# Optimization experiments

Hardware: AMD Instinct MI355X
Metric: run time of the kernel (lower is better)

Reference implementation:

```python
import jax, jax.numpy as jnp
import numpy as np

# --- static config (matches init_kwargs) ---
T, V, D, H = 4096, 32000, 1024, 16
DH = D // H                      # rope/head dim = 64
E, CAP, K, HOPS = 8, 1024, 2, 3  # non-identity experts, capacity, top-k, hops
MLP = 4 * D
ROPE_BASE = 10000.0
ATTN_IDX = np.array([0, 2, 4, 6])  # experts built with i%2==0 -> Attention
FFN_IDX = np.array([1, 3, 5, 7])   # i%2==1 -> FeedForward
EPS = 1e-6


def rope_cos_sin(t, dh, base):
    inv = 1.0 / (base ** (jnp.arange(0, dh, 2, dtype=jnp.float32) / dh))
    ang = jnp.arange(t, dtype=jnp.float32)[:, None] * inv[None, :]  # [T, dh/2]
    ang = jnp.concatenate([ang, ang], axis=-1)                      # [T, dh]
    return jnp.cos(ang), jnp.sin(ang)


def rotate_half(x):
    h = x.shape[-1] // 2
    return jnp.concatenate([-x[..., h:], x[..., :h]], axis=-1)


def topk_mask(logits, k):
    # boolean [T, E_total] mask of per-row top-k
    _, idx = jax.lax.top_k(logits, k)
    hard = jax.nn.one_hot(idx, logits.shape[-1]).sum(axis=-2)
    return hard.astype(bool)


def capacity_select(mask_te, gate_te, capacity):
    # mask_te: [T,E] bool, gate_te: [T,E] float -> slot [E,C,T], kept [E,T]
    m = mask_te.T                                   # [E, T]
    g = jnp.where(m, gate_te.T, -jnp.inf)           # [E, T]
    cap = int(min(capacity, g.shape[1]))
    _, top_idx = jax.lax.top_k(g, cap)              # [E, C]
    Ee, C = top_idx.shape
    slot = jnp.zeros((Ee, C, g.shape[1]), g.dtype)
    slot = slot.at[jnp.arange(Ee)[:, None], jnp.arange(C)[None, :], top_idx].set(1.0)
    slot = slot * m[:, None, :]                     # drop -inf fill slots
    kept = slot.sum(1).astype(bool)                 # [E, T]
    return slot, kept


def rms_norm(x, w):
    return x * jax.lax.rsqrt(jnp.mean(x * x, axis=-1, keepdims=True) + EPS) * w


def attention_group(x, cos_r, sin_r, wq, wk, wv, wo):
    # x: [G,C,D]; cos_r/sin_r: [G,C,DH]; weights: [G,D,D]
    G, C, _ = x.shape
    q = jnp.einsum('gcd,gde->gce', x, wq).reshape(G, C, H, DH)
    k = jnp.einsum('gcd,gde->gce', x, wk).reshape(G, C, H, DH)
    v = jnp.einsum('gcd,gde->gce', x, wv).reshape(G, C, H, DH)
    c = cos_r[:, :, None, :]
    s = sin_r[:, :, None, :]
    q = q * c + rotate_half(q) * s
    k = k * c + rotate_half(k) * s
    scores = jnp.einsum('gqhd,gkhd->ghqk', q, k) / np.sqrt(DH).astype(np.float32)
    attn = jax.nn.softmax(scores, axis=-1)
    out = jnp.einsum('ghqk,gkhd->gqhd', attn, v).reshape(G, C, D)
    return jnp.einsum('gcd,gde->gce', out, wo)


def ffn_group(x, w1, w2):
    # x: [G,C,D]; w1: [G,D,MLP]; w2: [G,MLP,D]
    return jnp.einsum('gcf,gfd->gcd', jax.nn.gelu(jnp.einsum('gcd,gdf->gcf', x, w1)), w2)


def dna_forward(ids, embed_w, router_w, wq, wk, wv, wo, w1, w2, ln_w):
    h = embed_w[ids]                                     # [T, D]
    cos, sin = rope_cos_sin(T, DH, ROPE_BASE)            # [T, DH]
    for hop in range(HOPS):
        logits = h @ router_w[hop].T                     # [T, E+1]
        probs = jax.nn.softmax(logits, axis=-1)
        mask_full = topk_mask(logits, K)                 # [T, E+1]
        probs_tr = probs[:, :-1]                         # [T, E]
        mask_tr = mask_full[:, :-1]
        slot, kept = capacity_select(mask_tr, probs_tr, CAP)  # [E,C,T], [E,T]
        # dispatch
        xin = jnp.einsum('ect,td->ecd', slot, h)          # [E, C, D]
        cos_r = jnp.einsum('ect,td->ecd', slot, cos)      # [E, C, DH]
        sin_r = jnp.einsum('ect,td->ecd', slot, sin)
        # grouped expert execution (stacked params, vectorized over group dim)
        attn_out = attention_group(xin[ATTN_IDX], cos_r[ATTN_IDX], sin_r[ATTN_IDX],
                                   wq, wk, wv, wo)        # [4, C, D]
        ffn_out = ffn_group(xin[FFN_IDX], w1, w2)         # [4, C, D]
        expert_out = jnp.zeros((E, CAP, D), h.dtype)
        expert_out = expert_out.at[ATTN_IDX].set(attn_out).at[FFN_IDX].set(ffn_out)
        # combine
        combine_w = jnp.where(kept.T, probs_tr, 0.0)      # [T, E]
        rho = combine_w.sum(axis=1, keepdims=True)        # [T, 1]
        combine = jnp.einsum('ecd,ect,et->td', expert_out, slot, combine_w.T)
        h = h + combine - rho * h
    return rms_norm(h, ln_w)


def setup_inputs() -> dict:
    key = jax.random.key(0)
    ks = jax.random.split(key, 10)
    sc = 0.02
    return {
        'ids': jax.random.randint(ks[0], (T,), 0, V),
        'embed_w': jax.random.normal(ks[1], (V, D), jnp.float32) * sc,
        'router_w': jax.random.normal(ks[2], (HOPS, E + 1, D), jnp.float32) * sc,
        'wq': jax.random.normal(ks[3], (4, D, D), jnp.float32) * sc,
        'wk': jax.random.normal(ks[4], (4, D, D), jnp.float32) * sc,
        'wv': jax.random.normal(ks[5], (4, D, D), jnp.float32) * sc,
        'wo': jax.random.normal(ks[6], (4, D, D), jnp.float32) * sc,
        'w1': jax.random.normal(ks[7], (4, D, MLP), jnp.float32) * sc,
        'w2': jax.random.normal(ks[8], (4, MLP, D), jnp.float32) * sc,
        'ln_w': jnp.ones((D,), jnp.float32),
    }


def reference(ids, embed_w, router_w, wq, wk, wv, wo, w1, w2, ln_w):
    return dna_forward(ids, embed_w, router_w, wq, wk, wv, wo, w1, w2, ln_w)
```

## Files before the change

kernel.cpp:

```cpp
#include <hip/hip_runtime.h>
#include <math.h>

#define T_ 4096
#define D_ 1024
#define H_ 16
#define DH_ 64
#define E_ 8
#define CAP_ 1024
#define MLP_ 4096
#define HOPS_ 3

__global__ __launch_bounds__(256) void embed_kernel(
    const int* __restrict__ ids, const float* __restrict__ ew, float* __restrict__ h)
{
  const int t = blockIdx.x;
  const int id = ids[t];
  const int c = threadIdx.x * 4;
  *(float4*)(h + (size_t)t * D_ + c) = *(const float4*)(ew + (size_t)id * D_ + c);
}

__global__ __launch_bounds__(64) void router_kernel(
    const float* __restrict__ h, const float* __restrict__ rw,
    float* __restrict__ probs, float* __restrict__ gmask)
{
  const int t = blockIdx.x;
  const int lane = threadIdx.x;
  __shared__ float hs[D_];
  #pragma unroll
  for (int j = 0; j < 4; ++j)
    *(float4*)&hs[lane * 4 + j * 256] = *(const float4*)(h + (size_t)t * D_ + lane * 4 + j * 256);
  __syncthreads();
  float l9[9];
  #pragma unroll
  for (int e = 0; e < 9; ++e) {
    float s = 0.0f;
    for (int i = lane; i < D_; i += 64) s += hs[i] * rw[e * D_ + i];
    #pragma unroll
    for (int off = 32; off > 0; off >>= 1) s += __shfl_down(s, off);
    l9[e] = s;
  }
  if (lane == 0) {
    float m = l9[0];
    #pragma unroll
    for (int e = 1; e < 9; ++e) m = fmaxf(m, l9[e]);
    float sum = 0.0f;
    float ex[9];
    #pragma unroll
    for (int e = 0; e < 9; ++e) { ex[e] = expf(l9[e] - m); sum += ex[e]; }
    const float inv = 1.0f / sum;
    int b1 = 0;
    #pragma unroll
    for (int e = 1; e < 9; ++e) if (l9[e] > l9[b1]) b1 = e;
    int b2 = (b1 == 0) ? 1 : 0;
    #pragma unroll
    for (int e = 0; e < 9; ++e) if (e != b1 && e != b2 && l9[e] > l9[b2]) b2 = e;
    #pragma unroll
    for (int e = 0; e < 8; ++e) {
      const float pe = ex[e] * inv;
      probs[t * 8 + e] = pe;
      gmask[(size_t)e * T_ + t] = (e == b1 || e == b2) ? pe : -1e30f;
    }
  }
}

__global__ __launch_bounds__(256) void zero_kernel(float* __restrict__ rho, int* __restrict__ cnt)
{
  const int i = blockIdx.x * 256 + threadIdx.x;
  if (i < T_) rho[i] = 0.0f;
  if (i < E_) cnt[i] = 0;
}

__global__ __launch_bounds__(256) void zeroeo_kernel(float* __restrict__ eo)
{
  const size_t i = ((size_t)blockIdx.x * 256 + threadIdx.x) * 4;
  float4 z; z.x = z.y = z.z = z.w = 0.0f;
  *(float4*)(eo + i) = z;
}

__global__ __launch_bounds__(256) void select_kernel(
    const float* __restrict__ gmask, const float* __restrict__ probs,
    int* __restrict__ idx, int* __restrict__ cnt, float* __restrict__ rho)
{
  __shared__ float row[T_];
  const int e = blockIdx.y;
  const int tid = threadIdx.x;
  const float* gr = gmask + (size_t)e * T_;
  #pragma unroll
  for (int j = 0; j < 16; ++j) row[tid + 256 * j] = gr[tid + 256 * j];
  __syncthreads();
  const int t = blockIdx.x * 256 + tid;
  const float g = row[t];
  if (g > -1e29f) {
    int rank = 0;
    for (int tt = 0; tt < T_; ++tt) {
      const float gg = row[tt];
      rank += (gg > g) || (gg == g && tt < t);
    }
    if (rank < CAP_) {
      const int pos = atomicAdd(&cnt[e], 1);
      idx[e * CAP_ + pos] = t;
      atomicAdd(&rho[t], probs[t * 8 + e]);
    }
  }
}

typedef __bf16 bf16x8 __attribute__((ext_vector_type(8)));
typedef float f32x4v __attribute__((ext_vector_type(4)));

union FragU { uint2 u2[2]; bf16x8 v; };

__device__ __forceinline__ unsigned pack_hi2(unsigned u0, unsigned u1)
{
  return (u0 >> 16) | (u1 & 0xFFFF0000u);
}

__device__ __forceinline__ void split8(const float4 a, const float4 b, FragU& h, FragU& l)
{
  const float f[8] = {a.x, a.y, a.z, a.w, b.x, b.y, b.z, b.w};
  unsigned hu[8], lu[8];
  #pragma unroll
  for (int i = 0; i < 8; ++i) {
    const unsigned u = __float_as_uint(f[i]);
    const float lo = f[i] - __uint_as_float(u & 0xFFFF0000u);
    hu[i] = u; lu[i] = __float_as_uint(lo);
  }
  h.u2[0].x = pack_hi2(hu[0], hu[1]); h.u2[0].y = pack_hi2(hu[2], hu[3]);
  h.u2[1].x = pack_hi2(hu[4], hu[5]); h.u2[1].y = pack_hi2(hu[6], hu[7]);
  l.u2[0].x = pack_hi2(lu[0], lu[1]); l.u2[0].y = pack_hi2(lu[2], lu[3]);
  l.u2[1].x = pack_hi2(lu[4], lu[5]); l.u2[1].y = pack_hi2(lu[6], lu[7]);
}

__device__ __forceinline__ void lds_load16(const void* g, void* l)
{
  __builtin_amdgcn_global_load_lds(
      (const __attribute__((address_space(1))) unsigned int*)g,
      (__attribute__((address_space(3))) unsigned int*)l, 16, 0, 0);
}

__device__ __forceinline__ float gelu_tanh(float x)
{
  const float x3 = x * x * x;
  return 0.5f * x * (1.0f + tanhf(0.7978845608028654f * (x + 0.044715f * x3)));
}

__global__ __launch_bounds__(256) void gather_kernel(
    const float* __restrict__ h, const int* __restrict__ idx, const int* __restrict__ cnt,
    unsigned short* __restrict__ xinp)
{
  const int c = blockIdx.x, e = blockIdx.y;
  const int c4 = threadIdx.x * 4;
  unsigned short* dst = xinp + ((size_t)e * CAP_ + c) * 2 * D_;
  if (c < cnt[e]) {
    const int t = idx[e * CAP_ + c];
    const float4 x = *(const float4*)(h + (size_t)t * D_ + c4);
    const float f[4] = {x.x, x.y, x.z, x.w};
    unsigned hu[4], lu[4];
    #pragma unroll
    for (int j = 0; j < 4; ++j) {
      const unsigned u = __float_as_uint(f[j]);
      const float lo = f[j] - __uint_as_float(u & 0xFFFF0000u);
      hu[j] = u; lu[j] = __float_as_uint(lo);
    }
    uint2 hp, lp;
    hp.x = pack_hi2(hu[0], hu[1]); hp.y = pack_hi2(hu[2], hu[3]);
    lp.x = pack_hi2(lu[0], lu[1]); lp.y = pack_hi2(lu[2], lu[3]);
    *(uint2*)(dst + c4) = hp;
    *(uint2*)(dst + D_ + c4) = lp;
  } else {
    uint2 z; z.x = 0u; z.y = 0u;
    *(uint2*)(dst + c4) = z;
    *(uint2*)(dst + D_ + c4) = z;
  }
}

__global__ __launch_bounds__(256) void convw_kernel(
    const float* __restrict__ W, unsigned short* __restrict__ out, int K, int N)
{
  const float* Wp = W + (size_t)blockIdx.z * K * N;
  unsigned short* op = out + (size_t)blockIdx.z * N * 2 * K;
  const int k0 = blockIdx.y * 64, n0 = blockIdx.x * 64;
  __shared__ float tile[64][65];
  const int tr = threadIdx.x >> 6;
  const int tc = threadIdx.x & 63;
  #pragma unroll
  for (int it = 0; it < 16; ++it) {
    const int r = it * 4 + tr;
    tile[r][tc] = Wp[(size_t)(k0 + r) * N + n0 + tc];
  }
  __syncthreads();
  #pragma unroll
  for (int it = 0; it < 16; ++it) {
    const int n = it * 4 + tr;
    const float f = tile[tc][n];
    const unsigned u = __float_as_uint(f);
    const float lo = f - __uint_as_float(u & 0xFFFF0000u);
    op[(size_t)(n0 + n) * 2 * K + k0 + tc] = (unsigned short)(u >> 16);
    op[(size_t)(n0 + n) * 2 * K + K + k0 + tc] = (unsigned short)(__float_as_uint(lo) >> 16);
  }
}

template <int EPI>
__device__ __forceinline__ void gemm_bf16_core(
    const unsigned short* __restrict__ A, const unsigned short* __restrict__ B,
    void* __restrict__ Cv, int N, int K, int kc0, int nkc, int m0, int n0)
{
  __shared__ unsigned short As[128 * 64];
  __shared__ unsigned short Bs[128 * 64];

  const int tid = threadIdx.x;
  const int lane = tid & 63;
  const int w = tid >> 6;
  const int wm = w >> 1, wn = w & 1;
  const int quad = lane >> 4, l15 = lane & 15;
  const size_t K2 = (size_t)2 * K;

  f32x4v acc[4][4];
  #pragma unroll
  for (int i = 0; i < 4; ++i)
    #pragma unroll
    for (int j = 0; j < 4; ++j) { acc[i][j][0] = 0.f; acc[i][j][1] = 0.f; acc[i][j][2] = 0.f; acc[i][j][3] = 0.f; }

  const int r0 = tid >> 3;
  const int pc = tid & 7;

  for (int kc = kc0; kc < kc0 + nkc; ++kc) {
    const int kb = kc * 32;
    __syncthreads();
    #pragma unroll
    for (int i = 0; i < 4; ++i) {
      const int row = r0 + i * 32;
      const int lc = pc ^ (row & 7);
      const int goff = (lc < 4) ? (kb + lc * 8) : (K + kb + (lc - 4) * 8);
      lds_load16(A + (size_t)(m0 + row) * K2 + goff, &As[(tid + i * 256) * 8]);
    }
    #pragma unroll
    for (int i = 0; i < 4; ++i) {
      const int row = r0 + i * 32;
      const int lc = pc ^ (row & 7);
      const int goff = (lc < 4) ? (kb + lc * 8) : (K + kb + (lc - 4) * 8);
      lds_load16(B + (size_t)(n0 + row) * K2 + goff, &Bs[(tid + i * 256) * 8]);
    }
    __syncthreads();

    FragU fah[4], fbh[4], fbl[4], fal[4];
    #pragma unroll
    for (int i = 0; i < 4; ++i) {
      const int row = wm * 64 + i * 16 + l15;
      const unsigned short* pr = &As[row * 64 + ((quad ^ (row & 7)) * 8)];
      fah[i].u2[0] = *(const uint2*)pr; fah[i].u2[1] = *(const uint2*)(pr + 4);
    }
    #pragma unroll
    for (int j = 0; j < 4; ++j) {
      const int row = wn * 64 + j * 16 + l15;
      const unsigned short* pr = &Bs[row * 64 + ((quad ^ (row & 7)) * 8)];
      fbh[j].u2[0] = *(const uint2*)pr; fbh[j].u2[1] = *(const uint2*)(pr + 4);
    }
    #pragma unroll
    for (int i = 0; i < 4; ++i)
      #pragma unroll
      for (int j = 0; j < 4; ++j)
        acc[i][j] = __builtin_amdgcn_mfma_f32_16x16x32_bf16(fah[i].v, fbh[j].v, acc[i][j], 0, 0, 0);
    #pragma unroll
    for (int j = 0; j < 4; ++j) {
      const int row = wn * 64 + j * 16 + l15;
      const unsigned short* pr = &Bs[row * 64 + (((quad + 4) ^ (row & 7)) * 8)];
      fbl[j].u2[0] = *(const uint2*)pr; fbl[j].u2[1] = *(const uint2*)(pr + 4);
    }
    #pragma unroll
    for (int i = 0; i < 4; ++i)
      #pragma unroll
      for (int j = 0; j < 4; ++j)
        acc[i][j] = __builtin_amdgcn_mfma_f32_16x16x32_bf16(fah[i].v, fbl[j].v, acc[i][j], 0, 0, 0);
    #pragma unroll
    for (int i = 0; i < 4; ++i) {
      const int row = wm * 64 + i * 16 + l15;
      const unsigned short* pr = &As[row * 64 + (((quad + 4) ^ (row & 7)) * 8)];
      fal[i].u2[0] = *(const uint2*)pr; fal[i].u2[1] = *(const uint2*)(pr + 4);
    }
    #pragma unroll
    for (int i = 0; i < 4; ++i)
      #pragma unroll
      for (int j = 0; j < 4; ++j)
        acc[i][j] = __builtin_amdgcn_mfma_f32_16x16x32_bf16(fal[i].v, fbh[j].v, acc[i][j], 0, 0, 0);
  }

  #pragma unroll
  for (int i = 0; i < 4; ++i)
    #pragma unroll
    for (int j = 0; j < 4; ++j) {
      const int n = n0 + wn * 64 + j * 16 + l15;
      #pragma unroll
      for (int r = 0; r < 4; ++r) {
        const int m = m0 + wm * 64 + i * 16 + quad * 4 + r;
        const float v = acc[i][j][r];
        if (EPI == 0) {
          ((float*)Cv)[(size_t)m * N + n] = v;
        } else if (EPI == 2) {
          atomicAdd(&((float*)Cv)[(size_t)m * N + n], v);
        } else {
          const float gv = gelu_tanh(v);
          const unsigned u = __float_as_uint(gv);
          const float lo = gv - __uint_as_float(u & 0xFFFF0000u);
          unsigned short* C = (unsigned short*)Cv;
          C[(size_t)m * 2 * N + n] = (unsigned short)(u >> 16);
          C[(size_t)m * 2 * N + N + n] = (unsigned short)(__float_as_uint(lo) >> 16);
        }
      }
    }
}

template <int EPI, int SK>
__global__ __launch_bounds__(256, 2) void gemm_bf16_k(
    const unsigned short* __restrict__ Ab, const unsigned short* __restrict__ Bb,
    void* __restrict__ Cb, int N, int K, long sA, long sB, long sC)
{
  const int nx = gridDim.x, ny = gridDim.y;
  const int total = nx * ny * gridDim.z;
  int flat = blockIdx.x + nx * (blockIdx.y + ny * blockIdx.z);
  int s = (flat & 7) * (total >> 3) + (flat >> 3);
  const int bx = s % nx; s /= nx;
  const int by = s % ny;
  const int z = s / ny;

  const int g = z / SK, sp = z - g * SK;
  const unsigned short* A = Ab + (size_t)g * sA;
  const unsigned short* B = Bb + (size_t)g * sB;
  void* C;
  if (EPI == 1) C = (void*)((unsigned short*)Cb + (size_t)g * sC);
  else          C = (void*)((float*)Cb + (size_t)g * sC);
  const int nkc = (K / 32) / SK;
  gemm_bf16_core<EPI>(A, B, C, N, K, sp * nkc, nkc, by * 128, bx * 128);
}

__global__ __launch_bounds__(256, 2) void gemm_qkv_bf16(
    const unsigned short* __restrict__ xinp,
    const unsigned short* __restrict__ wqp, const unsigned short* __restrict__ wkp,
    const unsigned short* __restrict__ wvp,
    float* __restrict__ qb, float* __restrict__ kb, float* __restrict__ vb)
{
  const int nx = gridDim.x, ny = gridDim.y;
  const int total = nx * ny * gridDim.z;
  int flat = blockIdx.x + nx * (blockIdx.y + ny * blockIdx.z);
  int s = (flat & 7) * (total >> 3) + (flat >> 3);
  const int bx = s % nx; s /= nx;
  const int by = s % ny;
  const int z = s / ny;

  const int g = z & 3;
  const int which = z >> 2;
  const unsigned short* A = xinp + (size_t)(2 * g) * CAP_ * 2 * D_;
  const unsigned short* B = ((which == 0) ? wqp : (which == 1) ? wkp : wvp) + (size_t)g * D_ * 2 * D_;
  float* C = ((which == 0) ? qb : (which == 1) ? kb : vb) + (size_t)g * CAP_ * D_;
  gemm_bf16_core<0>(A, B, (void*)C, D_, D_, 0, 32, by * 128, bx * 128);
}

__global__ __launch_bounds__(256) void rope_kernel(
    float* __restrict__ q, float* __restrict__ k,
    const int* __restrict__ idx, const int* __restrict__ cnt)
{
  const int c = blockIdx.x, g = blockIdx.y;
  const int e = 2 * g;
  if (c >= cnt[e]) return;
  const int t = idx[e * CAP_ + c];
  const int tid = threadIdx.x;
  const int hh = tid >> 4;
  const int pp = tid & 15;
  const size_t base = ((size_t)g * CAP_ + c) * D_ + hh * DH_;
  const float tf = (float)t;
  #pragma unroll
  for (int u = 0; u < 2; ++u) {
    const int i = pp * 2 + u;
    const float invf = (float)::pow(10000.0, -(double)i / 32.0);
    const float ang = tf * invf;
    const float cs = (float)::cos((double)ang);
    const float sn = (float)::sin((double)ang);
    const float q0 = q[base + i], q1 = q[base + i + 32];
    q[base + i]      = q0 * cs - q1 * sn;
    q[base + i + 32] = q1 * cs + q0 * sn;
    const float k0 = k[base + i], k1 = k[base + i + 32];
    k[base + i]      = k0 * cs - k1 * sn;
    k[base + i + 32] = k1 * cs + k0 * sn;
  }
}

#define FBQ 128
#define LDK 68
#define LDQ 72

__global__ __launch_bounds__(256, 2) void flash_mfma(
    const float* __restrict__ qg, const float* __restrict__ kg,
    const float* __restrict__ vg, unsigned short* __restrict__ og)
{
  const int g = blockIdx.z, hh = blockIdx.y, qt = blockIdx.x;
  const size_t base = (size_t)g * CAP_ * D_ + hh * DH_;
  const float* Q = qg + base;
  const float* Kp = kg + base;
  const float* Vp = vg + base;
  unsigned short* Ob = og + (size_t)g * CAP_ * 2 * D_ + hh * DH_;

  __shared__ __align__(16) char lds_raw[69632];
  unsigned short* Kh  = (unsigned short*)lds_raw;
  unsigned short* Kl  = Kh  + 64 * LDK;
  unsigned short* Vth = Kl  + 64 * LDK;
  unsigned short* Vtl = Vth + 64 * LDK;
  unsigned short* Ph  = Vtl + 64 * LDK;
  unsigned short* Pl  = Ph  + FBQ * LDK;
  float* Qs = (float*)lds_raw;

  const int tid = threadIdx.x;
  const int lane = tid & 63;
  const int w = tid >> 6;
  const int quad = lane >> 4;
  const int l15 = lane & 15;

  #pragma unroll
  for (int it = 0; it < 8; ++it) {
    const int row = it * 16 + (tid >> 4);
    const int c4 = (tid & 15) * 4;
    *(float4*)&Qs[row * LDQ + c4] = *(const float4*)(Q + (size_t)(qt * FBQ + row) * D_ + c4);
  }
  __syncthreads();
  FragU qf[2][2][2];
  #pragma unroll
  for (int rs = 0; rs < 2; ++rs)
    #pragma unroll
    for (int ks = 0; ks < 2; ++ks) {
      const float* p0 = &Qs[(w * 32 + rs * 16 + l15) * LDQ + ks * 32 + quad * 8];
      const float4 f0 = *(const float4*)p0;
      const float4 f1 = *(const float4*)(p0 + 4);
      split8(f0, f1, qf[rs][ks][0], qf[rs][ks][1]);
    }
  __syncthreads();

  f32x4v acc[2][4];
  float m_r[2][4], l_r[2][4];
  #pragma unroll
  for (int rs = 0; rs < 2; ++rs)
    #pragma unroll
    for (int r = 0; r < 4; ++r) { m_r[rs][r] = -1e30f; l_r[rs][r] = 0.0f; }
  #pragma unroll
  for (int rs = 0; rs < 2; ++rs)
    #pragma unroll
    for (int dt = 0; dt < 4; ++dt) { acc[rs][dt][0] = 0.f; acc[rs][dt][1] = 0.f; acc[rs][dt][2] = 0.f; acc[rs][dt][3] = 0.f; }

  for (int kt = 0; kt < 16; ++kt) {
    __syncthreads();
    #pragma unroll
    for (int it = 0; it < 4; ++it) {
      const int r = it * 16 + (tid >> 4);
      const int c4 = (tid & 15) * 4;
      const float4 kv = *(const float4*)(Kp + (size_t)(kt * 64 + r) * D_ + c4);
      {
        const unsigned u0 = __float_as_uint(kv.x), u1 = __float_as_uint(kv.y);
        const unsigned u2 = __float_as_uint(kv.z), u3 = __float_as_uint(kv.w);
        const float l0 = kv.x - __uint_as_float(u0 & 0xFFFF0000u);
        const float l1 = kv.y - __uint_as_float(u1 & 0xFFFF0000u);
        const float l2 = kv.z - __uint_as_float(u2 & 0xFFFF0000u);
        const float l3 = kv.w - __uint_as_float(u3 & 0xFFFF0000u);
        uint2 hp, lp;
        hp.x = pack_hi2(u0, u1); hp.y = pack_hi2(u2, u3);
        lp.x = pack_hi2(__float_as_uint(l0), __float_as_uint(l1));
        lp.y = pack_hi2(__float_as_uint(l2), __float_as_uint(l3));
        *(uint2*)&Kh[r * LDK + c4] = hp;
        *(uint2*)&Kl[r * LDK + c4] = lp;
      }
      const float4 vv = *(const float4*)(Vp + (size_t)(kt * 64 + r) * D_ + c4);
      const float vf[4] = {vv.x, vv.y, vv.z, vv.w};
      #pragma unroll
      for (int u = 0; u < 4; ++u) {
        const unsigned uu = __float_as_uint(vf[u]);
        const float lo = vf[u] - __uint_as_float(uu & 0xFFFF0000u);
        Vth[(c4 + u) * LDK + r] = (unsigned short)(uu >> 16);
        Vtl[(c4 + u) * LDK + r] = (unsigned short)(__float_as_uint(lo) >> 16);
      }
    }
    __syncthreads();
    f32x4v sfr[2][4];
    #pragma unroll
    for (int rs = 0; rs < 2; ++rs)
      #pragma unroll
      for (int j = 0; j < 4; ++j) {
        f32x4v s; s[0] = 0.f; s[1] = 0.f; s[2] = 0.f; s[3] = 0.f;
        #pragma unroll
        for (int ks = 0; ks < 2; ++ks) {
          FragU kh, kl;
          const unsigned short* pk = &Kh[(j * 16 + l15) * LDK + ks * 32 + quad * 8];
          const unsigned short* pl = &Kl[(j * 16 + l15) * LDK + ks * 32 + quad * 8];
          kh.u2[0] = *(const uint2*)pk; kh.u2[1] = *(const uint2*)(pk + 4);
          kl.u2[0] = *(const uint2*)pl; kl.u2[1] = *(const uint2*)(pl + 4);
          s = __builtin_amdgcn_mfma_f32_16x16x32_bf16(qf[rs][ks][0].v, kh.v, s, 0, 0, 0);
          s = __builtin_amdgcn_mfma_f32_16x16x32_bf16(qf[rs][ks][0].v, kl.v, s, 0, 0, 0);
          s = __builtin_amdgcn_mfma_f32_16x16x32_bf16(qf[rs][ks][1].v, kh.v, s, 0, 0, 0);
        }
        sfr[rs][j] = s;
      }
    #pragma unroll
    for (int rs = 0; rs < 2; ++rs) {
      #pragma unroll
      for (int r = 0; r < 4; ++r) {
        float s0 = sfr[rs][0][r] * 0.125f;
        float s1 = sfr[rs][1][r] * 0.125f;
        float s2 = sfr[rs][2][r] * 0.125f;
        float s3 = sfr[rs][3][r] * 0.125f;
        float mx = fmaxf(fmaxf(s0, s1), fmaxf(s2, s3));
        #pragma unroll
        for (int o = 1; o < 16; o <<= 1) mx = fmaxf(mx, __shfl_xor(mx, o));
        const float nm = fmaxf(m_r[rs][r], mx);
        const float al = __expf(m_r[rs][r] - nm);
        m_r[rs][r] = nm;
        const float p0 = __expf(s0 - nm);
        const float p1 = __expf(s1 - nm);
        const float p2 = __expf(s2 - nm);
        const float p3 = __expf(s3 - nm);
        float rsum = p0 + p1 + p2 + p3;
        #pragma unroll
        for (int o = 1; o < 16; o <<= 1) rsum += __shfl_xor(rsum, o);
        l_r[rs][r] = l_r[rs][r] * al + rsum;
        #pragma unroll
        for (int dt = 0; dt < 4; ++dt) acc[rs][dt][r] *= al;
        const int row = w * 32 + rs * 16 + quad * 4 + r;
        const float pv[4] = {p0, p1, p2, p3};
        #pragma unroll
        for (int j = 0; j < 4; ++j) {
          const unsigned u = __float_as_uint(pv[j]);
          const float lo = pv[j] - __uint_as_float(u & 0xFFFF0000u);
          Ph[row * LDK + j * 16 + l15] = (unsigned short)(u >> 16);
          Pl[row * LDK + j * 16 + l15] = (unsigned short)(__float_as_uint(lo) >> 16);
        }
      }
    }
    __syncthreads();
    FragU pf[2][2][2];
    #pragma unroll
    for (int rs = 0; rs < 2; ++rs)
      #pragma unroll
      for (int ks = 0; ks < 2; ++ks) {
        const unsigned short* ph = &Ph[(w * 32 + rs * 16 + l15) * LDK + ks * 32 + quad * 8];
        const unsigned short* pl = &Pl[(w * 32 + rs * 16 + l15) * LDK + ks * 32 + quad * 8];
        pf[rs][ks][0].u2[0] = *(const uint2*)ph; pf[rs][ks][0].u2[1] = *(const uint2*)(ph + 4);
        pf[rs][ks][1].u2[0] = *(const uint2*)pl; pf[rs][ks][1].u2[1] = *(const uint2*)(pl + 4);
      }
    #pragma unroll
    for (int dt = 0; dt < 4; ++dt)
      #pragma unroll
      for (int ks = 0; ks < 2; ++ks) {
        FragU vh, vl;
        const unsigned short* pv_ = &Vth[(dt * 16 + l15) * LDK + ks * 32 + quad * 8];
        const unsigned short* pl_ = &Vtl[(dt * 16 + l15) * LDK + ks * 32 + quad * 8];
        vh.u2[0] = *(const uint2*)pv_; vh.u2[1] = *(const uint2*)(pv_ + 4);
        vl.u2[0] = *(const uint2*)pl_; vl.u2[1] = *(const uint2*)(pl_ + 4);
        #pragma unroll
        for (int rs = 0; rs < 2; ++rs) {
          acc[rs][dt] = __builtin_amdgcn_mfma_f32_16x16x32_bf16(pf[rs][ks][0].v, vh.v, acc[rs][dt], 0, 0, 0);
          acc[rs][dt] = __builtin_amdgcn_mfma_f32_16x16x32_bf16(pf[rs][ks][0].v, vl.v, acc[rs][dt], 0, 0, 0);
          acc[rs][dt] = __builtin_amdgcn_mfma_f32_16x16x32_bf16(pf[rs][ks][1].v, vh.v, acc[rs][dt], 0, 0, 0);
        }
      }
  }
  #pragma unroll
  for (int rs = 0; rs < 2; ++rs)
    #pragma unroll
    for (int r = 0; r < 4; ++r) {
      const float inv = 1.0f / l_r[rs][r];
      const int row = qt * FBQ + w * 32 + rs * 16 + quad * 4 + r;
      #pragma unroll
      for (int dt = 0; dt < 4; ++dt) {
        const float v = acc[rs][dt][r] * inv;
        const unsigned u = __float_as_uint(v);
        const float lo = v - __uint_as_float(u & 0xFFFF0000u);
        Ob[(size_t)row * 2 * D_ + dt * 16 + l15] = (unsigned short)(u >> 16);
        Ob[(size_t)row * 2 * D_ + D_ + dt * 16 + l15] = (unsigned short)(__float_as_uint(lo) >> 16);
      }
    }
}

__global__ __launch_bounds__(256) void initnew_kernel(
    const float* __restrict__ h, const float* __restrict__ rho, float* __restrict__ hn)
{
  const int t = blockIdx.x;
  const float f = 1.0f - rho[t];
  const int c = threadIdx.x * 4;
  float4 x = *(const float4*)(h + (size_t)t * D_ + c);
  x.x *= f; x.y *= f; x.z *= f; x.w *= f;
  *(float4*)(hn + (size_t)t * D_ + c) = x;
}

__global__ __launch_bounds__(256) void scatter_kernel(
    const float* __restrict__ eo, const int* __restrict__ idx, const int* __restrict__ cnt,
    const float* __restrict__ probs, float* __restrict__ hn)
{
  const int c = blockIdx.x, e = blockIdx.y;
  if (c >= cnt[e]) return;
  const int t = idx[e * CAP_ + c];
  const float w = probs[t * 8 + e];
  const float* src = eo + ((size_t)e * CAP_ + c) * D_;
  float* dst = hn + (size_t)t * D_;
  const int c4 = threadIdx.x * 4;
  #pragma unroll
  for (int j = 0; j < 4; ++j) atomicAdd(dst + c4 + j, src[c4 + j] * w);
}

__global__ __launch_bounds__(256) void rms_kernel(
    const float* __restrict__ h, const float* __restrict__ w, float* __restrict__ out)
{
  const int t = blockIdx.x;
  const int c = threadIdx.x * 4;
  const float4 x = *(const float4*)(h + (size_t)t * D_ + c);
  float ss = x.x * x.x + x.y * x.y + x.z * x.z + x.w * x.w;
  #pragma unroll
  for (int off = 32; off > 0; off >>= 1) ss += __shfl_down(ss, off);
  __shared__ float wsum[4];
  __shared__ float sscale;
  const int lane = threadIdx.x & 63, wv = threadIdx.x >> 6;
  if (lane == 0) wsum[wv] = ss;
  __syncthreads();
  if (threadIdx.x == 0) {
    const float s = wsum[0] + wsum[1] + wsum[2] + wsum[3];
    sscale = 1.0f / sqrtf(s * (1.0f / (float)D_) + 1e-6f);
  }
  __syncthreads();
  const float sc = sscale;
  const float4 w4 = *(const float4*)(w + c);
  float4 o;
  o.x = x.x * sc * w4.x; o.y = x.y * sc * w4.y; o.z = x.z * sc * w4.z; o.w = x.w * sc * w4.w;
  *(float4*)(out + (size_t)t * D_ + c) = o;
}

extern "C" void kernel_launch(void* const* d_in, const int* in_sizes, int n_in,
                              void* d_out, int out_size, void* d_ws, size_t ws_size,
                              hipStream_t stream)
{
  (void)in_sizes; (void)n_in; (void)out_size; (void)ws_size;
  const int* ids = (const int*)d_in[0];
  const float* embed_w = (const float*)d_in[1];
  const float* router_w = (const float*)d_in[2];
  const float* wq = (const float*)d_in[3];
  const float* wk = (const float*)d_in[4];
  const float* wv = (const float*)d_in[5];
  const float* wo = (const float*)d_in[6];
  const float* w1 = (const float*)d_in[7];
  const float* w2 = (const float*)d_in[8];
  const float* lnw = (const float*)d_in[9];
  float* out = (float*)d_out;

  float* p = (float*)d_ws;
  const size_t TD = (size_t)T_ * D_;
  float* hA = p;    p += TD;
  float* hB = p;    p += TD;
  float* probs = p; p += (size_t)T_ * E_;
  float* gmask = p; p += (size_t)E_ * T_;
  float* rho = p;   p += T_;
  int* idx = (int*)p;   p += E_ * CAP_;
  int* cnt = (int*)p;   p += 16;
  float* eo = p;   p += (size_t)E_ * CAP_ * D_;
  float* qb = p;   p += (size_t)4 * CAP_ * D_;
  float* kb = p;   p += (size_t)4 * CAP_ * D_;
  float* vb = p;   p += (size_t)4 * CAP_ * D_;
  unsigned short* aob = (unsigned short*)p; p += (size_t)4 * CAP_ * D_;
  unsigned short* midp = (unsigned short*)qb;
  unsigned short* xinp = (unsigned short*)p; p += (size_t)E_ * CAP_ * D_;
  unsigned short* wqp = (unsigned short*)p; p += (size_t)4 * D_ * D_;
  unsigned short* wkp = (unsigned short*)p; p += (size_t)4 * D_ * D_;
  unsigned short* wvp = (unsigned short*)p; p += (size_t)4 * D_ * D_;
  unsigned short* wop = (unsigned short*)p; p += (size_t)4 * D_ * D_;
  unsigned short* w1p = (unsigned short*)p; p += (size_t)4 * D_ * MLP_;
  unsigned short* w2p = (unsigned short*)p; p += (size_t)4 * D_ * MLP_;

  convw_kernel<<<dim3(D_ / 64, D_ / 64, 4), 256, 0, stream>>>(wq, wqp, D_, D_);
  convw_kernel<<<dim3(D_ / 64, D_ / 64, 4), 256, 0, stream>>>(wk, wkp, D_, D_);
  convw_kernel<<<dim3(D_ / 64, D_ / 64, 4), 256, 0, stream>>>(wv, wvp, D_, D_);
  convw_kernel<<<dim3(D_ / 64, D_ / 64, 4), 256, 0, stream>>>(wo, wop, D_, D_);
  convw_kernel<<<dim3(MLP_ / 64, D_ / 64, 4), 256, 0, stream>>>(w1, w1p, D_, MLP_);
  convw_kernel<<<dim3(D_ / 64, MLP_ / 64, 4), 256, 0, stream>>>(w2, w2p, MLP_, D_);

  embed_kernel<<<T_, 256, 0, stream>>>(ids, embed_w, hA);
  float* cur = hA;
  float* nxt = hB;
  for (int hop = 0; hop < HOPS_; ++hop) {
    router_kernel<<<T_, 64, 0, stream>>>(cur, router_w + (size_t)hop * 9 * D_, probs, gmask);
    zero_kernel<<<16, 256, 0, stream>>>(rho, cnt);
    select_kernel<<<dim3(16, 8), 256, 0, stream>>>(gmask, probs, idx, cnt, rho);
    gather_kernel<<<dim3(CAP_, E_), 256, 0, stream>>>(cur, idx, cnt, xinp);
    gemm_qkv_bf16<<<dim3(D_ / 128, CAP_ / 128, 12), 256, 0, stream>>>(xinp, wqp, wkp, wvp, qb, kb, vb);
    rope_kernel<<<dim3(CAP_, 4), 256, 0, stream>>>(qb, kb, idx, cnt);
    flash_mfma<<<dim3(CAP_ / FBQ, 16, 4), 256, 0, stream>>>(qb, kb, vb, aob);
    zeroeo_kernel<<<8192, 256, 0, stream>>>(eo);
    gemm_bf16_k<2, 4><<<dim3(D_ / 128, CAP_ / 128, 16), 256, 0, stream>>>(
        aob, wop, (void*)eo, D_, D_,
        (long)CAP_ * 2 * D_, (long)D_ * 2 * D_, (long)2 * CAP_ * D_);
    gemm_bf16_k<1, 1><<<dim3(MLP_ / 128, CAP_ / 128, 4), 256, 0, stream>>>(
        xinp + (size_t)CAP_ * 2 * D_, w1p, (void*)midp, MLP_, D_,
        (long)2 * CAP_ * 2 * D_, (long)MLP_ * 2 * D_, (long)CAP_ * 2 * MLP_);
    gemm_bf16_k<2, 4><<<dim3(D_ / 128, CAP_ / 128, 16), 256, 0, stream>>>(
        midp, w2p, (void*)(eo + (size_t)CAP_ * D_), D_, MLP_,
        (long)CAP_ * 2 * MLP_, (long)D_ * 2 * MLP_, (long)2 * CAP_ * D_);
    initnew_kernel<<<T_, 256, 0, stream>>>(cur, rho, nxt);
    scatter_kernel<<<dim3(CAP_, E_), 256, 0, stream>>>(eo, idx, cnt, probs, nxt);
    float* tmp = cur; cur = nxt; nxt = tmp;
  }
  rms_kernel<<<T_, 256, 0, stream>>>(cur, lnw, out);
}
```

Baseline: 2.724 ms.

## Use 256x256 double-buffered GEMM tiles with prefetch interleaved into MFMA phases

Replaces the 128x128, 256-thread bf16-split GEMM core with a 256x256, 512-thread version. The new core double-buffers A and B in LDS and issues the next K-chunk's global-to-LDS loads between the six MFMA phases. It also raises wave priority around the MFMA blocks and cuts per-iteration synchronisation to plain barriers. The aim is to hide load latency and raise arithmetic intensity per tile. In exchange, LDS use rises to 128KB per block and grids shrink (e.g. 192 blocks for QKV), so occupancy and CU fill may drop.

```diff
diff --git a/kernel.cpp b/kernel.cpp
--- a/kernel.cpp
+++ b/kernel.cpp
@@ -200,98 +200,100 @@
 }
 
 template <int EPI>
-__device__ __forceinline__ void gemm_bf16_core(
+__device__ __forceinline__ void gemm_bf16_core256(
     const unsigned short* __restrict__ A, const unsigned short* __restrict__ B,
     void* __restrict__ Cv, int N, int K, int kc0, int nkc, int m0, int n0)
 {
-  __shared__ unsigned short As[128 * 64];
-  __shared__ unsigned short Bs[128 * 64];
+  __shared__ unsigned short As[2][256 * 64];
+  __shared__ unsigned short Bs[2][256 * 64];
 
   const int tid = threadIdx.x;
   const int lane = tid & 63;
   const int w = tid >> 6;
-  const int wm = w >> 1, wn = w & 1;
+  const int wm = w >> 2, wn = w & 3;
   const int quad = lane >> 4, l15 = lane & 15;
   const size_t K2 = (size_t)2 * K;
 
-  f32x4v acc[4][4];
-  #pragma unroll
-  for (int i = 0; i < 4; ++i)
+  f32x4v acc[8][4];
+  #pragma unroll
+  for (int i = 0; i < 8; ++i)
     #pragma unroll
     for (int j = 0; j < 4; ++j) { acc[i][j][0] = 0.f; acc[i][j][1] = 0.f; acc[i][j][2] = 0.f; acc[i][j][3] = 0.f; }
 
   const int r0 = tid >> 3;
   const int pc = tid & 7;
 
-  for (int kc = kc0; kc < kc0 + nkc; ++kc) {
-    const int kb = kc * 32;
-    __syncthreads();
-    #pragma unroll
-    for (int i = 0; i < 4; ++i) {
-      const int row = r0 + i * 32;
+  {
+    const int kb = kc0 * 32;
+    #pragma unroll
+    for (int p = 0; p < 4; ++p) {
+      const int row = p * 64 + r0;
       const int lc = pc ^ (row & 7);
       const int goff = (lc < 4) ? (kb + lc * 8) : (K + kb + (lc - 4) * 8);
-      lds_load16(A + (size_t)(m0 + row) * K2 + goff, &As[(tid + i * 256) * 8]);
-    }
-    #pragma unroll
-    for (int i = 0; i < 4; ++i) {
-      const int row = r0 + i * 32;
-      const int lc = pc ^ (row & 7);
-      const int goff = (lc < 4) ? (kb + lc * 8) : (K + kb + (lc - 4) * 8);
-      lds_load16(B + (size_t)(n0 + row) * K2 + goff, &Bs[(tid + i * 256) * 8]);
-    }
-    __syncthreads();
-
-    FragU fah[4], fbh[4], fbl[4], fal[4];
-    #pragma unroll
-    for (int i = 0; i < 4; ++i) {
-      const int row = wm * 64 + i * 16 + l15;
-      const unsigned short* pr = &As[row * 64 + ((quad ^ (row & 7)) * 8)];
-      fah[i].u2[0] = *(const uint2*)pr; fah[i].u2[1] = *(const uint2*)(pr + 4);
-    }
-    #pragma unroll
-    for (int j = 0; j < 4; ++j) {
-      const int row = wn * 64 + j * 16 + l15;
-      const unsigned short* pr = &Bs[row * 64 + ((quad ^ (row & 7)) * 8)];
-      fbh[j].u2[0] = *(const uint2*)pr; fbh[j].u2[1] = *(const uint2*)(pr + 4);
-    }
-    #pragma unroll
-    for (int i = 0; i < 4; ++i)
-      #pragma unroll
-      for (int j = 0; j < 4; ++j)
-        acc[i][j] = __builtin_amdgcn_mfma_f32_16x16x32_bf16(fah[i].v, fbh[j].v, acc[i][j], 0, 0, 0);
-    #pragma unroll
-    for (int j = 0; j < 4; ++j) {
-      const int row = wn * 64 + j * 16 + l15;
-      const unsigned short* pr = &Bs[row * 64 + (((quad + 4) ^ (row & 7)) * 8)];
-      fbl[j].u2[0] = *(const uint2*)pr; fbl[j].u2[1] = *(const uint2*)(pr + 4);
-    }
-    #pragma unroll
-    for (int i = 0; i < 4; ++i)
-      #pragma unroll
-      for (int j = 0; j < 4; ++j)
-        acc[i][j] = __builtin_amdgcn_mfma_f32_16x16x32_bf16(fah[i].v, fbl[j].v, acc[i][j], 0, 0, 0);
-    #pragma unroll
-    for (int i = 0; i < 4; ++i) {
-      const int row = wm * 64 + i * 16 + l15;
-      const unsigned short* pr = &As[row * 64 + (((quad + 4) ^ (row & 7)) * 8)];
-      fal[i].u2[0] = *(const uint2*)pr; fal[i].u2[1] = *(const uint2*)(pr + 4);
-    }
-    #pragma unroll
-    for (int i = 0; i < 4; ++i)
-      #pragma unroll
-      for (int j = 0; j < 4; ++j)
-        acc[i][j] = __builtin_amdgcn_mfma_f32_16x16x32_bf16(fal[i].v, fbh[j].v, acc[i][j], 0, 0, 0);
-  }
-
-  #pragma unroll
-  for (int i = 0; i < 4; ++i)
+      lds_load16(A + (size_t)(m0 + row) * K2 + goff, (void*)&As[0][row * 64 + pc * 8]);
+      lds_load16(B + (size_t)(n0 + row) * K2 + goff, (void*)&Bs[0][row * 64 + pc * 8]);
+    }
+    asm volatile("s_waitcnt vmcnt(0)" ::: "memory");
+    __builtin_amdgcn_s_barrier();
+  }
+
+  const unsigned short* Ac = &As[0][0];
+  const unsigned short* Bc = &Bs[0][0];
+  unsigned short* An = &As[1][0];
+  unsigned short* Bn = &Bs[1][0];
+
+  for (int kc = kc0; kc < kc0 + nkc; ++kc) {
+    const bool nx = (kc + 1 < kc0 + nkc);
+    const int kbn = (kc + 1) * 32;
+    #pragma unroll
+    for (int p = 0; p < 6; ++p) {
+      const int pi = p >> 1;
+      const int hf = p & 1;
+      const int ao = (pi == 2) ? 4 : 0;
+      const int bo = (pi == 1) ? 4 : 0;
+      FragU fa[4], fb[4];
+      #pragma unroll
+      for (int i = 0; i < 4; ++i) {
+        const int row = wm * 128 + (hf * 4 + i) * 16 + l15;
+        const unsigned short* pr = &Ac[row * 64 + (((quad + ao) ^ (row & 7)) * 8)];
+        fa[i].u2[0] = *(const uint2*)pr; fa[i].u2[1] = *(const uint2*)(pr + 4);
+      }
+      #pragma unroll
+      for (int j = 0; j < 4; ++j) {
+        const int row = wn * 64 + j * 16 + l15;
+        const unsigned short* pr = &Bc[row * 64 + (((quad + bo) ^ (row & 7)) * 8)];
+        fb[j].u2[0] = *(const uint2*)pr; fb[j].u2[1] = *(const uint2*)(pr + 4);
+      }
+      if (nx && p < 4) {
+        const int row = p * 64 + r0;
+        const int lc = pc ^ (row & 7);
+        const int goff = (lc < 4) ? (kbn + lc * 8) : (K + kbn + (lc - 4) * 8);
+        lds_load16(A + (size_t)(m0 + row) * K2 + goff, An + row * 64 + pc * 8);
+        lds_load16(B + (size_t)(n0 + row) * K2 + goff, Bn + row * 64 + pc * 8);
+      }
+      __builtin_amdgcn_s_barrier();
+      __builtin_amdgcn_s_setprio(1);
+      #pragma unroll
+      for (int i = 0; i < 4; ++i)
+        #pragma unroll
+        for (int j = 0; j < 4; ++j)
+          acc[hf * 4 + i][j] = __builtin_amdgcn_mfma_f32_16x16x32_bf16(fa[i].v, fb[j].v, acc[hf * 4 + i][j], 0, 0, 0);
+      __builtin_amdgcn_s_setprio(0);
+      if (p == 5 && nx) asm volatile("s_waitcnt vmcnt(0)" ::: "memory");
+      __builtin_amdgcn_s_barrier();
+    }
+    const unsigned short* t1 = Ac; Ac = An; An = (unsigned short*)t1;
+    const unsigned short* t2 = Bc; Bc = Bn; Bn = (unsigned short*)t2;
+  }
+
+  #pragma unroll
+  for (int i = 0; i < 8; ++i)
     #pragma unroll
     for (int j = 0; j < 4; ++j) {
       const int n = n0 + wn * 64 + j * 16 + l15;
       #pragma unroll
       for (int r = 0; r < 4; ++r) {
-        const int m = m0 + wm * 64 + i * 16 + quad * 4 + r;
+        const int m = m0 + wm * 128 + i * 16 + quad * 4 + r;
         const float v = acc[i][j][r];
         if (EPI == 0) {
           ((float*)Cv)[(size_t)m * N + n] = v;
@@ -310,7 +312,7 @@
 }
 
 template <int EPI, int SK>
-__global__ __launch_bounds__(256, 2) void gemm_bf16_k(
+__global__ __launch_bounds__(512, 2) void gemm_bf16_k(
     const unsigned short* __restrict__ Ab, const unsigned short* __restrict__ Bb,
     void* __restrict__ Cb, int N, int K, long sA, long sB, long sC)
 {
@@ -329,10 +331,10 @@
   if (EPI == 1) C = (void*)((unsigned short*)Cb + (size_t)g * sC);
   else          C = (void*)((float*)Cb + (size_t)g * sC);
   const int nkc = (K / 32) / SK;
-  gemm_bf16_core<EPI>(A, B, C, N, K, sp * nkc, nkc, by * 128, bx * 128);
-}
-
-__global__ __launch_bounds__(256, 2) void gemm_qkv_bf16(
+  gemm_bf16_core256<EPI>(A, B, C, N, K, sp * nkc, nkc, by * 256, bx * 256);
+}
+
+__global__ __launch_bounds__(512, 2) void gemm_qkv_bf16(
     const unsigned short* __restrict__ xinp,
     const unsigned short* __restrict__ wqp, const unsigned short* __restrict__ wkp,
     const unsigned short* __restrict__ wvp,
@@ -351,7 +353,7 @@
   const unsigned short* A = xinp + (size_t)(2 * g) * CAP_ * 2 * D_;
   const unsigned short* B = ((which == 0) ? wqp : (which == 1) ? wkp : wvp) + (size_t)g * D_ * 2 * D_;
   float* C = ((which == 0) ? qb : (which == 1) ? kb : vb) + (size_t)g * CAP_ * D_;
-  gemm_bf16_core<0>(A, B, (void*)C, D_, D_, 0, 32, by * 128, bx * 128);
+  gemm_bf16_core256<0>(A, B, (void*)C, D_, D_, 0, 32, by * 256, bx * 256);
 }
 
 __global__ __launch_bounds__(256) void rope_kernel(
@@ -681,17 +683,17 @@
     zero_kernel<<<16, 256, 0, stream>>>(rho, cnt);
     select_kernel<<<dim3(16, 8), 256, 0, stream>>>(gmask, probs, idx, cnt, rho);
     gather_kernel<<<dim3(CAP_, E_), 256, 0, stream>>>(cur, idx, cnt, xinp);
-    gemm_qkv_bf16<<<dim3(D_ / 128, CAP_ / 128, 12), 256, 0, stream>>>(xinp, wqp, wkp, wvp, qb, kb, vb);
+    gemm_qkv_bf16<<<dim3(D_ / 256, CAP_ / 256, 12), 512, 0, stream>>>(xinp, wqp, wkp, wvp, qb, kb, vb);
     rope_kernel<<<dim3(CAP_, 4), 256, 0, stream>>>(qb, kb, idx, cnt);
     flash_mfma<<<dim3(CAP_ / FBQ, 16, 4), 256, 0, stream>>>(qb, kb, vb, aob);
     zeroeo_kernel<<<8192, 256, 0, stream>>>(eo);
-    gemm_bf16_k<2, 4><<<dim3(D_ / 128, CAP_ / 128, 16), 256, 0, stream>>>(
+    gemm_bf16_k<2, 4><<<dim3(D_ / 256, CAP_ / 256, 16), 512, 0, stream>>>(
         aob, wop, (void*)eo, D_, D_,
         (long)CAP_ * 2 * D_, (long)D_ * 2 * D_, (long)2 * CAP_ * D_);
-    gemm_bf16_k<1, 1><<<dim3(MLP_ / 128, CAP_ / 128, 4), 256, 0, stream>>>(
+    gemm_bf16_k<1, 1><<<dim3(MLP_ / 256, CAP_ / 256, 4), 512, 0, stream>>>(
         xinp + (size_t)CAP_ * 2 * D_, w1p, (void*)midp, MLP_, D_,
         (long)2 * CAP_ * 2 * D_, (long)MLP_ * 2 * D_, (long)CAP_ * 2 * MLP_);
-    gemm_bf16_k<2, 4><<<dim3(D_ / 128, CAP_ / 128, 16), 256, 0, stream>>>(
+    gemm_bf16_k<2, 4><<<dim3(D_ / 256, CAP_ / 256, 16), 512, 0, stream>>>(
         midp, w2p, (void*)(eo + (size_t)CAP_ * D_), D_, MLP_,
         (long)CAP_ * 2 * MLP_, (long)D_ * 2 * MLP_, (long)2 * CAP_ * D_);
     initnew_kernel<<<T_, 256, 0, stream>>>(cur, rho, nxt);
```

After: 3.180 ms. 1.17x slower.

## Double-buffer LDS tiles in bf16 GEMM core and precompute RoPE cos/sin table

Applied to the files above, without the earlier changes.

The GEMM core now uses two LDS buffers so the global-to-LDS loads for the next k-chunk are issued before the MFMAs on the current chunk, overlapping memory latency with compute and dropping one barrier per iteration. RoPE cos/sin values, previously computed in double precision on every call and every hop, are computed once into a table and read by the rope kernel. The double buffer doubles LDS use per block, which may lower occupancy. The table adds a global read per element in place of the arithmetic.

```diff
diff --git a/kernel.cpp b/kernel.cpp
--- a/kernel.cpp
+++ b/kernel.cpp
@@ -75,6 +75,17 @@
   const size_t i = ((size_t)blockIdx.x * 256 + threadIdx.x) * 4;
   float4 z; z.x = z.y = z.z = z.w = 0.0f;
   *(float4*)(eo + i) = z;
+}
+
+__global__ __launch_bounds__(256) void rope_tab_kernel(float* __restrict__ tab)
+{
+  const int idx = blockIdx.x * 256 + threadIdx.x;
+  const int t = idx >> 5;
+  const int i = idx & 31;
+  const float invf = (float)::pow(10000.0, -(double)i / 32.0);
+  const float ang = (float)t * invf;
+  tab[idx * 2 + 0] = (float)::cos((double)ang);
+  tab[idx * 2 + 1] = (float)::sin((double)ang);
 }
 
 __global__ __launch_bounds__(256) void select_kernel(
@@ -204,8 +215,8 @@
     const unsigned short* __restrict__ A, const unsigned short* __restrict__ B,
     void* __restrict__ Cv, int N, int K, int kc0, int nkc, int m0, int n0)
 {
-  __shared__ unsigned short As[128 * 64];
-  __shared__ unsigned short Bs[128 * 64];
+  __shared__ unsigned short As[2][128 * 64];
+  __shared__ unsigned short Bs[2][128 * 64];
 
   const int tid = threadIdx.x;
   const int lane = tid & 63;
@@ -223,36 +234,46 @@
   const int r0 = tid >> 3;
   const int pc = tid & 7;
 
-  for (int kc = kc0; kc < kc0 + nkc; ++kc) {
-    const int kb = kc * 32;
-    __syncthreads();
+  {
+    const int kb = kc0 * 32;
+    const int lcp = pc ^ (r0 & 7);
+    const int goff0 = (lcp < 4) ? (kb + lcp * 8) : (K + kb + (lcp - 4) * 8);
     #pragma unroll
     for (int i = 0; i < 4; ++i) {
       const int row = r0 + i * 32;
-      const int lc = pc ^ (row & 7);
-      const int goff = (lc < 4) ? (kb + lc * 8) : (K + kb + (lc - 4) * 8);
-      lds_load16(A + (size_t)(m0 + row) * K2 + goff, &As[(tid + i * 256) * 8]);
-    }
-    #pragma unroll
-    for (int i = 0; i < 4; ++i) {
-      const int row = r0 + i * 32;
-      const int lc = pc ^ (row & 7);
-      const int goff = (lc < 4) ? (kb + lc * 8) : (K + kb + (lc - 4) * 8);
-      lds_load16(B + (size_t)(n0 + row) * K2 + goff, &Bs[(tid + i * 256) * 8]);
-    }
-    __syncthreads();
-
+      lds_load16(A + (size_t)(m0 + row) * K2 + goff0, (void*)&As[0][(tid + i * 256) * 8]);
+      lds_load16(B + (size_t)(n0 + row) * K2 + goff0, (void*)&Bs[0][(tid + i * 256) * 8]);
+    }
+    asm volatile("s_waitcnt vmcnt(0)" ::: "memory");
+    __builtin_amdgcn_s_barrier();
+  }
+
+  for (int kc = kc0; kc < kc0 + nkc; ++kc) {
+    const int cb = (kc - kc0) & 1;
+    if (kc + 1 < kc0 + nkc) {
+      const int kb = (kc + 1) * 32;
+      const int lcp = pc ^ (r0 & 7);
+      const int goff0 = (lcp < 4) ? (kb + lcp * 8) : (K + kb + (lcp - 4) * 8);
+      #pragma unroll
+      for (int i = 0; i < 4; ++i) {
+        const int row = r0 + i * 32;
+        lds_load16(A + (size_t)(m0 + row) * K2 + goff0, (void*)&As[cb ^ 1][(tid + i * 256) * 8]);
+        lds_load16(B + (size_t)(n0 + row) * K2 + goff0, (void*)&Bs[cb ^ 1][(tid + i * 256) * 8]);
+      }
+    }
+    const unsigned short* Ac = &As[cb][0];
+    const unsigned short* Bc = &Bs[cb][0];
     FragU fah[4], fbh[4], fbl[4], fal[4];
     #pragma unroll
     for (int i = 0; i < 4; ++i) {
       const int row = wm * 64 + i * 16 + l15;
-      const unsigned short* pr = &As[row * 64 + ((quad ^ (row & 7)) * 8)];
+      const unsigned short* pr = &Ac[row * 64 + ((quad ^ (row & 7)) * 8)];
       fah[i].u2[0] = *(const uint2*)pr; fah[i].u2[1] = *(const uint2*)(pr + 4);
     }
     #pragma unroll
     for (int j = 0; j < 4; ++j) {
       const int row = wn * 64 + j * 16 + l15;
-      const unsigned short* pr = &Bs[row * 64 + ((quad ^ (row & 7)) * 8)];
+      const unsigned short* pr = &Bc[row * 64 + ((quad ^ (row & 7)) * 8)];
       fbh[j].u2[0] = *(const uint2*)pr; fbh[j].u2[1] = *(const uint2*)(pr + 4);
     }
     #pragma unroll
@@ -263,7 +284,7 @@
     #pragma unroll
     for (int j = 0; j < 4; ++j) {
       const int row = wn * 64 + j * 16 + l15;
-      const unsigned short* pr = &Bs[row * 64 + (((quad + 4) ^ (row & 7)) * 8)];
+      const unsigned short* pr = &Bc[row * 64 + (((quad + 4) ^ (row & 7)) * 8)];
       fbl[j].u2[0] = *(const uint2*)pr; fbl[j].u2[1] = *(const uint2*)(pr + 4);
     }
     #pragma unroll
@@ -274,7 +295,7 @@
     #pragma unroll
     for (int i = 0; i < 4; ++i) {
       const int row = wm * 64 + i * 16 + l15;
-      const unsigned short* pr = &As[row * 64 + (((quad + 4) ^ (row & 7)) * 8)];
+      const unsigned short* pr = &Ac[row * 64 + (((quad + 4) ^ (row & 7)) * 8)];
       fal[i].u2[0] = *(const uint2*)pr; fal[i].u2[1] = *(const uint2*)(pr + 4);
     }
     #pragma unroll
@@ -282,6 +303,8 @@
       #pragma unroll
       for (int j = 0; j < 4; ++j)
         acc[i][j] = __builtin_amdgcn_mfma_f32_16x16x32_bf16(fal[i].v, fbh[j].v, acc[i][j], 0, 0, 0);
+    asm volatile("s_waitcnt vmcnt(0)" ::: "memory");
+    __builtin_amdgcn_s_barrier();
   }
 
   #pragma unroll
@@ -356,7 +379,8 @@
 
 __global__ __launch_bounds__(256) void rope_kernel(
     float* __restrict__ q, float* __restrict__ k,
-    const int* __restrict__ idx, const int* __restrict__ cnt)
+    const int* __restrict__ idx, const int* __restrict__ cnt,
+    const float* __restrict__ tab)
 {
   const int c = blockIdx.x, g = blockIdx.y;
   const int e = 2 * g;
@@ -366,14 +390,11 @@
   const int hh = tid >> 4;
   const int pp = tid & 15;
   const size_t base = ((size_t)g * CAP_ + c) * D_ + hh * DH_;
-  const float tf = (float)t;
   #pragma unroll
   for (int u = 0; u < 2; ++u) {
     const int i = pp * 2 + u;
-    const float invf = (float)::pow(10000.0, -(double)i / 32.0);
-    const float ang = tf * invf;
-    const float cs = (float)::cos((double)ang);
-    const float sn = (float)::sin((double)ang);
+    const float cs = tab[(t * 32 + i) * 2 + 0];
+    const float sn = tab[(t * 32 + i) * 2 + 1];
     const float q0 = q[base + i], q1 = q[base + i + 32];
     q[base + i]      = q0 * cs - q1 * sn;
     q[base + i + 32] = q1 * cs + q0 * sn;
@@ -652,6 +673,7 @@
   float* rho = p;   p += T_;
   int* idx = (int*)p;   p += E_ * CAP_;
   int* cnt = (int*)p;   p += 16;
+  float* rct = p;  p += (size_t)T_ * 64;
   float* eo = p;   p += (size_t)E_ * CAP_ * D_;
   float* qb = p;   p += (size_t)4 * CAP_ * D_;
   float* kb = p;   p += (size_t)4 * CAP_ * D_;
@@ -672,6 +694,7 @@
   convw_kernel<<<dim3(D_ / 64, D_ / 64, 4), 256, 0, stream>>>(wo, wop, D_, D_);
   convw_kernel<<<dim3(MLP_ / 64, D_ / 64, 4), 256, 0, stream>>>(w1, w1p, D_, MLP_);
   convw_kernel<<<dim3(D_ / 64, MLP_ / 64, 4), 256, 0, stream>>>(w2, w2p, MLP_, D_);
+  rope_tab_kernel<<<T_ * 32 / 256, 256, 0, stream>>>(rct);
 
   embed_kernel<<<T_, 256, 0, stream>>>(ids, embed_w, hA);
   float* cur = hA;
@@ -682,7 +705,7 @@
     select_kernel<<<dim3(16, 8), 256, 0, stream>>>(gmask, probs, idx, cnt, rho);
     gather_kernel<<<dim3(CAP_, E_), 256, 0, stream>>>(cur, idx, cnt, xinp);
     gemm_qkv_bf16<<<dim3(D_ / 128, CAP_ / 128, 12), 256, 0, stream>>>(xinp, wqp, wkp, wvp, qb, kb, vb);
-    rope_kernel<<<dim3(CAP_, 4), 256, 0, stream>>>(qb, kb, idx, cnt);
+    rope_kernel<<<dim3(CAP_, 4), 256, 0, stream>>>(qb, kb, idx, cnt, rct);
     flash_mfma<<<dim3(CAP_ / FBQ, 16, 4), 256, 0, stream>>>(qb, kb, vb, aob);
     zeroeo_kernel<<<8192, 256, 0, stream>>>(eo);
     gemm_bf16_k<2, 4><<<dim3(D_ / 128, CAP_ / 128, 16), 256, 0, stream>>>(
```

Result: slower. 2.832 ms (+3.9%).
